# Performance work log

Hardware: AMD Instinct MI355X
Metric: run time of the kernel (lower is better)

Reference implementation:

```python
import jax, jax.numpy as jnp
import numpy as np

H = 1024
NS, NQ, S = 32, 64, 256
ADAPT_STEPS = 5


def _mlp_ln(x, W1, b1, W2, b2, g, be):
    # Linear -> ReLU -> Linear -> LayerNorm (dropout is identity in eval)
    h = jax.nn.relu(x @ W1 + b1) @ W2 + b2
    mu = h.mean(-1, keepdims=True)
    var = ((h - mu) ** 2).mean(-1, keepdims=True)
    return g * (h - mu) / jnp.sqrt(var + 1e-5) + be


def setup_inputs() -> dict:
    key = jax.random.key(0)
    ks = jax.random.split(key, 16)
    d = {}
    d['support_embeddings'] = jax.random.normal(ks[0], (NS, S, H), jnp.float32)
    d['query_embeddings'] = jax.random.normal(ks[1], (NQ, S, H), jnp.float32)
    d['support_labels'] = jax.random.randint(ks[2], (NS, S), 0, 3)
    w = lambda k, fi, fo: jax.random.normal(k, (fi, fo), jnp.float32) * (1.0 / np.sqrt(fi))
    # aspect_aware encoder
    d['aw_W1'] = w(ks[3], H, H); d['aw_b1'] = jnp.zeros((H,), jnp.float32)
    d['aw_W2'] = w(ks[4], H, H); d['aw_b2'] = jnp.zeros((H,), jnp.float32)
    d['aw_g'] = jnp.ones((H,), jnp.float32); d['aw_be'] = jnp.zeros((H,), jnp.float32)
    # aspect_contrastive encoder
    d['ct_W1'] = w(ks[5], H, H); d['ct_b1'] = jnp.zeros((H,), jnp.float32)
    d['ct_W2'] = w(ks[6], H, H); d['ct_b2'] = jnp.zeros((H,), jnp.float32)
    d['ct_g'] = jnp.ones((H,), jnp.float32); d['ct_be'] = jnp.zeros((H,), jnp.float32)
    # adaptation net (randomly-initialized 2-layer MLP in the torch code)
    d['ad_W1'] = w(ks[7], H, H); d['ad_b1'] = jnp.zeros((H,), jnp.float32)
    d['ad_W2'] = w(ks[8], H, H); d['ad_b2'] = jnp.zeros((H,), jnp.float32)
    # meta classifier
    d['cl_W1'] = w(ks[9], 2 * H, H); d['cl_b1'] = jnp.zeros((H,), jnp.float32)
    d['cl_W2'] = w(ks[10], H, 64); d['cl_b2'] = jnp.zeros((64,), jnp.float32)
    d['cl_W3'] = w(ks[11], 64, 3); d['cl_b3'] = jnp.zeros((3,), jnp.float32)
    return d


def reference(support_embeddings, query_embeddings, support_labels,
              aw_W1, aw_b1, aw_W2, aw_b2, aw_g, aw_be,
              ct_W1, ct_b1, ct_W2, ct_b2, ct_g, ct_be,
              ad_W1, ad_b1, ad_W2, ad_b2,
              cl_W1, cl_b1, cl_W2, cl_b2, cl_W3, cl_b3):
    # --- encode support set, build per-sentence aspect prototypes ---
    aw_s = _mlp_ln(support_embeddings, aw_W1, aw_b1, aw_W2, aw_b2, aw_g, aw_be)  # [NS,S,H]
    mask = (support_labels > 0).astype(aw_s.dtype)[..., None]                    # [NS,S,1]
    cnt = jnp.maximum(mask.sum(axis=1), 1.0)                                     # [NS,1]
    protos = (aw_s * mask).sum(axis=1) / cnt                                     # [NS,H] masked mean
    pn = protos / jnp.maximum(jnp.linalg.norm(protos, axis=-1, keepdims=True), 1e-8)

    # --- meta-adaptation: fused over all (query, token) pairs, 5 steps ---
    adapted = query_embeddings
    for _ in range(ADAPT_STEPS):
        qn = adapted / jnp.maximum(jnp.linalg.norm(adapted, axis=-1, keepdims=True), 1e-8)
        sims = jnp.einsum('qsh,ph->qsp', qn, pn)           # cosine similarities
        wts = jax.nn.softmax(sims, axis=-1)
        infl = jnp.einsum('qsp,ph->qsh', wts, protos)      # prototype influence
        adapted = jax.nn.relu((adapted + infl) @ ad_W1 + ad_b1) @ ad_W2 + ad_b2

    # --- classify adapted query tokens ---
    q_aw = _mlp_ln(adapted, aw_W1, aw_b1, aw_W2, aw_b2, aw_g, aw_be)
    q_ct = _mlp_ln(adapted, ct_W1, ct_b1, ct_W2, ct_b2, ct_g, ct_be)
    comb = jnp.concatenate([q_aw, q_ct], axis=-1)          # [NQ,S,2H]
    h = jax.nn.relu(comb @ cl_W1 + cl_b1)
    h = jax.nn.relu(h @ cl_W2 + cl_b2)
    preds = h @ cl_W3 + cl_b3                              # [NQ,S,3]
    return preds
```

## Files before the change

kernel.cpp:

```cpp
#include <hip/hip_runtime.h>
#include <hip/hip_bf16.h>

#define H 1024
#define NS 32
#define SS 256
#define T_Q 16384
#define M_S 8192

typedef __hip_bfloat16 bf16;
typedef short short8 __attribute__((ext_vector_type(8)));
typedef float floatx4 __attribute__((ext_vector_type(4)));

__device__ __forceinline__ float ldf(const bf16& v) { return __bfloat162float(v); }

__device__ __forceinline__ void split2(float v, bf16& h, bf16& l) {
  h = __float2bfloat16(v);
  l = __float2bfloat16(v - __bfloat162float(h));
}

__device__ __forceinline__ void gl2lds16(const void* g, void* l) {
  __builtin_amdgcn_global_load_lds(
      (const __attribute__((address_space(1))) unsigned int*)g,
      (__attribute__((address_space(3))) unsigned int*)l, 16, 0, 0);
}

__device__ __forceinline__ short8 ld8s(const bf16* p) { return *(const short8*)p; }

__global__ __launch_bounds__(256) void conv_split(const float* __restrict__ in,
                                                  bf16* __restrict__ oh,
                                                  bf16* __restrict__ ol, int n)
{
  int i = blockIdx.x * 256 + threadIdx.x;
  if (i < n) { bf16 h, l; split2(in[i], h, l); oh[i] = h; ol[i] = l; }
}

__global__ __launch_bounds__(256) void transpose_split(
    const float* __restrict__ W, bf16* __restrict__ Wh, bf16* __restrict__ Wl,
    int K, int N)
{
  __shared__ float t[32][33];
  int n0 = blockIdx.x * 32, k0 = blockIdx.y * 32;
  int tx = threadIdx.x & 31, ty = threadIdx.x >> 5;
#pragma unroll
  for (int i = 0; i < 32; i += 8)
    t[ty + i][tx] = W[(size_t)(k0 + ty + i) * N + (n0 + tx)];
  __syncthreads();
#pragma unroll
  for (int i = 0; i < 32; i += 8) {
    bf16 h, l; split2(t[tx][ty + i], h, l);
    size_t o = (size_t)(n0 + ty + i) * K + (k0 + tx);
    Wh[o] = h;
    if (Wl) Wl[o] = l;
  }
}

template<bool RELU, bool HASWL>
__global__ __launch_bounds__(512, 2) void gemm3p(
    const bf16* __restrict__ A0h, const bf16* __restrict__ A0l,
    const bf16* __restrict__ A1h, const bf16* __restrict__ A1l,
    const bf16* __restrict__ Wh,  const bf16* __restrict__ Wl,
    const float* __restrict__ bias,
    bf16* __restrict__ Ch, bf16* __restrict__ Cl,
    int M, int N, int K0, int Ktot)
{
  (void)M;
  __shared__ __align__(16) bf16 lds[2 * 32768];
  const int tid = threadIdx.x;
  const int w = tid >> 6, l = tid & 63;
  const int nbm = gridDim.x >> 2;
  const int lid = blockIdx.x;
  const int xcd = lid & 7, ib = lid >> 3;
  const int half = nbm >> 1;
  const int bn = xcd >> 1;
  const int bm = (xcd & 1) * half + ib;
  const int wr = w >> 2, wn = w & 3;
  const int m16 = l & 15, quad = l >> 4;
  const int srow = l & 15;
  const int scol = (l >> 4) * 8;
  const int la = l * 8;

  floatx4 acc[8][4];
#pragma unroll
  for (int i = 0; i < 8; i++)
#pragma unroll
    for (int j = 0; j < 4; j++) { acc[i][j][0]=0.f; acc[i][j][1]=0.f; acc[i][j][2]=0.f; acc[i][j][3]=0.f; }

  const size_t raB0 = (size_t)(bn * 256 + (2 * w)     * 16 + srow) * Ktot + scol;
  const size_t raB1 = (size_t)(bn * 256 + (2 * w + 1) * 16 + srow) * Ktot + scol;
  const int aT  = ((w >> 1) & 1) + ((w >> 1) >> 1) * 8;
  const int aLo = w & 1;
  const size_t raA = (size_t)(bm * 256 + aT * 16 + srow) * H + scol;
  const int aDst = (aLo ? 8192 : 0) + aT * 512;
  size_t raBt[3]; int bDst[3]; int bLo[3];
#pragma unroll
  for (int i = 0; i < 3; i++) {
    int j = w * 3 + i;
    int idx = j >> 1;
    int tb = (idx < 6) ? (idx + 2) : (idx + 4);
    bLo[i] = j & 1;
    raBt[i] = (size_t)(bm * 256 + tb * 16 + srow) * H + scol;
    bDst[i] = (bLo[i] ? 8192 : 0) + tb * 512;
  }

  auto stage_alpha = [&](int t) {
    const int k0 = t << 5;
    const bf16 *Ah_, *Al_; int ke;
    if (k0 < K0) { Ah_ = A0h; Al_ = A0l; ke = k0; }
    else         { Ah_ = A1h; Al_ = A1l; ke = k0 - K0; }
    bf16* buf = lds + (t & 1) * 32768;
    gl2lds16(Wh + raB0 + k0, buf + 16384 + (2 * w) * 512);
    gl2lds16(Wh + raB1 + k0, buf + 16384 + (2 * w + 1) * 512);
    if (HASWL) {
      gl2lds16(Wl + raB0 + k0, buf + 24576 + (2 * w) * 512);
      gl2lds16(Wl + raB1 + k0, buf + 24576 + (2 * w + 1) * 512);
    }
    gl2lds16((aLo ? Al_ : Ah_) + raA + ke, buf + aDst);
  };
  auto stage_beta = [&](int t) {
    const int k0 = t << 5;
    const bf16 *Ah_, *Al_; int ke;
    if (k0 < K0) { Ah_ = A0h; Al_ = A0l; ke = k0; }
    else         { Ah_ = A1h; Al_ = A1l; ke = k0 - K0; }
    bf16* buf = lds + (t & 1) * 32768;
#pragma unroll
    for (int i = 0; i < 3; i++)
      gl2lds16((bLo[i] ? Al_ : Ah_) + raBt[i] + ke, buf + bDst[i]);
  };

  stage_alpha(0);
  stage_beta(0);
  asm volatile("s_waitcnt vmcnt(0)" ::: "memory");
  __builtin_amdgcn_s_barrier();

  short8 bh[4], bl8[4];
  short8 s0h[2], s0l[2], s1h[2], s1l[2];
  {
    const bf16* bB = lds + 16384 + wn * 2048 + la;
#pragma unroll
    for (int nt = 0; nt < 4; nt++) bh[nt] = ld8s(bB + nt * 512);
    if (HASWL) {
#pragma unroll
      for (int nt = 0; nt < 4; nt++) bl8[nt] = ld8s(bB + 8192 + nt * 512);
    }
    const bf16* bA = lds + wr * 4096 + la;
    s0h[0] = ld8s(bA);        s0h[1] = ld8s(bA + 512);
    s0l[0] = ld8s(bA + 8192); s0l[1] = ld8s(bA + 8704);
  }

  const int nT = Ktot >> 5;

#define MM3(MI, AH, AL)                                                                            \
    _Pragma("unroll")                                                                              \
    for (int nt = 0; nt < 4; nt++) {                                                               \
      acc[MI][nt] = __builtin_amdgcn_mfma_f32_16x16x32_bf16(AH, bh[nt],  acc[MI][nt], 0, 0, 0);    \
      acc[MI][nt] = __builtin_amdgcn_mfma_f32_16x16x32_bf16(AL, bh[nt],  acc[MI][nt], 0, 0, 0);    \
      if (HASWL)                                                                                   \
        acc[MI][nt] = __builtin_amdgcn_mfma_f32_16x16x32_bf16(AH, bl8[nt], acc[MI][nt], 0, 0, 0);  \
    }

  for (int t = 0; t < nT; ++t) {
    const bf16* buf  = lds + (t & 1) * 32768;
    const bf16* nbuf = lds + ((t + 1) & 1) * 32768;
    const bf16* bA   = buf + wr * 4096 + la;
    const bf16* bAl  = bA + 8192;

    if (t + 1 < nT) stage_alpha(t + 1);
    s1h[0] = ld8s(bA + 1024);  s1h[1] = ld8s(bA + 1536);
    s1l[0] = ld8s(bAl + 1024); s1l[1] = ld8s(bAl + 1536);
    __builtin_amdgcn_s_setprio(1);
    MM3(0, s0h[0], s0l[0])
    MM3(1, s0h[1], s0l[1])
    __builtin_amdgcn_s_setprio(0);

    if (t + 1 < nT) stage_beta(t + 1);
    s0h[0] = ld8s(bA + 2048);  s0h[1] = ld8s(bA + 2560);
    s0l[0] = ld8s(bAl + 2048); s0l[1] = ld8s(bAl + 2560);
    __builtin_amdgcn_s_setprio(1);
    MM3(2, s1h[0], s1l[0])
    MM3(3, s1h[1], s1l[1])
    __builtin_amdgcn_s_setprio(0);

    s1h[0] = ld8s(bA + 3072);  s1h[1] = ld8s(bA + 3584);
    s1l[0] = ld8s(bAl + 3072); s1l[1] = ld8s(bAl + 3584);
    __builtin_amdgcn_s_setprio(1);
    MM3(4, s0h[0], s0l[0])
    MM3(5, s0h[1], s0l[1])
    __builtin_amdgcn_s_setprio(0);
    if (t + 1 < nT) asm volatile("s_waitcnt vmcnt(3)" ::: "memory");
    __builtin_amdgcn_s_barrier();

    __builtin_amdgcn_s_setprio(1);
    MM3(6, s1h[0], s1l[0])
    MM3(7, s1h[1], s1l[1])
    __builtin_amdgcn_s_setprio(0);
    if (t + 1 < nT) {
      const bf16* nbB = nbuf + 16384 + wn * 2048 + la;
      const bf16* nbA = nbuf + wr * 4096 + la;
#pragma unroll
      for (int nt = 0; nt < 4; nt++) bh[nt] = ld8s(nbB + nt * 512);
      if (HASWL) {
#pragma unroll
        for (int nt = 0; nt < 4; nt++) bl8[nt] = ld8s(nbB + 8192 + nt * 512);
      }
      s0h[0] = ld8s(nbA);        s0h[1] = ld8s(nbA + 512);
      s0l[0] = ld8s(nbA + 8192); s0l[1] = ld8s(nbA + 8704);
      asm volatile("s_waitcnt vmcnt(0)" ::: "memory");
    }
    __builtin_amdgcn_s_barrier();
  }
#undef MM3

#pragma unroll
  for (int mt = 0; mt < 8; mt++) {
#pragma unroll
    for (int nt = 0; nt < 4; nt++) {
      int row0 = bm * 256 + wr * 128 + mt * 16 + quad * 4;
      int col  = bn * 256 + wn * 64 + nt * 16 + m16;
      float bv = bias ? bias[col] : 0.f;
#pragma unroll
      for (int r = 0; r < 4; r++) {
        float v = acc[mt][nt][r] + bv;
        if (RELU) v = fmaxf(v, 0.f);
        bf16 h, lo; split2(v, h, lo);
        size_t o = (size_t)(row0 + r) * N + col;
        Ch[o] = h; Cl[o] = lo;
      }
    }
  }
}

__global__ __launch_bounds__(256) void ln_pair(
    bf16* __restrict__ hh, bf16* __restrict__ hl,
    const float* __restrict__ g, const float* __restrict__ be)
{
  int row = blockIdx.x;
  bf16* ph = hh + (size_t)row * H;
  bf16* pl = hl + (size_t)row * H;
  int tid = threadIdx.x;
  float v[4];
  float s = 0.f, sq = 0.f;
#pragma unroll
  for (int j = 0; j < 4; j++) {
    int hi = tid + 256 * j;
    v[j] = ldf(ph[hi]) + ldf(pl[hi]);
    s += v[j]; sq += v[j] * v[j];
  }
  __shared__ float rs[256], rq[256];
  rs[tid] = s; rq[tid] = sq; __syncthreads();
  for (int o = 128; o; o >>= 1) {
    if (tid < o) { rs[tid] += rs[tid + o]; rq[tid] += rq[tid + o]; }
    __syncthreads();
  }
  float mu   = rs[0] * (1.0f / H);
  float var  = rq[0] * (1.0f / H) - mu * mu;
  float rstd = rsqrtf(var + 1e-5f);
#pragma unroll
  for (int j = 0; j < 4; j++) {
    int hi = tid + 256 * j;
    bf16 h, l; split2(g[hi] * (v[j] - mu) * rstd + be[hi], h, l);
    ph[hi] = h; pl[hi] = l;
  }
}

__global__ __launch_bounds__(256) void proto_kernel(
    const bf16* __restrict__ eh, const bf16* __restrict__ el,
    const int* __restrict__ labels, float* __restrict__ protos_out)
{
  int p = blockIdx.x;
  int tid = threadIdx.x;
  __shared__ unsigned char lbl[SS];
  lbl[tid] = (labels[p * SS + tid] > 0) ? 1 : 0;
  __syncthreads();
  float acc[4] = {0.f, 0.f, 0.f, 0.f};
  int cnt = 0;
  const bf16* bh = eh + (size_t)p * SS * H;
  const bf16* bl = el + (size_t)p * SS * H;
  for (int s = 0; s < SS; s++) {
    if (lbl[s]) {
      cnt++;
      const bf16* rh = bh + (size_t)s * H;
      const bf16* rl = bl + (size_t)s * H;
#pragma unroll
      for (int j = 0; j < 4; j++)
        acc[j] += ldf(rh[tid + 256 * j]) + ldf(rl[tid + 256 * j]);
    }
  }
  float ic = 1.0f / fmaxf((float)cnt, 1.0f);
#pragma unroll
  for (int j = 0; j < 4; j++) protos_out[p * H + tid + 256 * j] = acc[j] * ic;
}

__global__ __launch_bounds__(256) void pn_kernel(
    const float* __restrict__ protos, bf16* __restrict__ pnh, bf16* __restrict__ pnl)
{
  int p = blockIdx.x;
  int tid = threadIdx.x;
  __shared__ float red[256];
  float v[4];
  float sq = 0.f;
#pragma unroll
  for (int j = 0; j < 4; j++) { v[j] = protos[p * H + tid + 256 * j]; sq += v[j] * v[j]; }
  red[tid] = sq; __syncthreads();
  for (int o = 128; o; o >>= 1) {
    if (tid < o) red[tid] += red[tid + o];
    __syncthreads();
  }
  float inv = 1.0f / fmaxf(sqrtf(red[0]), 1e-8f);
#pragma unroll
  for (int j = 0; j < 4; j++) {
    bf16 h, l; split2(v[j] * inv, h, l);
    pnh[p * H + tid + 256 * j] = h;
    pnl[p * H + tid + 256 * j] = l;
  }
}

__global__ __launch_bounds__(256) void rownorm_pair(
    const bf16* __restrict__ hh, const bf16* __restrict__ hl, float* __restrict__ rn)
{
  int row = blockIdx.x;
  int tid = threadIdx.x;
  const bf16* ph = hh + (size_t)row * H;
  const bf16* pl = hl + (size_t)row * H;
  float s = 0.f;
#pragma unroll
  for (int j = 0; j < 4; j++) {
    float v = ldf(ph[tid + 256 * j]) + ldf(pl[tid + 256 * j]);
    s += v * v;
  }
  __shared__ float rs[256];
  rs[tid] = s; __syncthreads();
  for (int o = 128; o; o >>= 1) {
    if (tid < o) rs[tid] += rs[tid + o];
    __syncthreads();
  }
  if (tid == 0) rn[row] = 1.0f / fmaxf(sqrtf(rs[0]), 1e-8f);
}

__global__ __launch_bounds__(256) void sims_mfma(
    const bf16* __restrict__ Ah, const bf16* __restrict__ Al,
    const bf16* __restrict__ Bh, const bf16* __restrict__ Bl,
    float* __restrict__ sims)
{
  __shared__ bf16 AsH[64 * 32];
  __shared__ bf16 AsL[64 * 32];
  __shared__ bf16 BsH[32 * 32];
  __shared__ bf16 BsL[32 * 32];
  const int tid = threadIdx.x;
  const int w = tid >> 6, l = tid & 63;
  const int bm0 = blockIdx.x * 64;
  const int m16 = l & 15, quad = l >> 4;
  const int sr = l >> 2;
  const int sc = (l & 3) * 8;

  floatx4 acc[2];
#pragma unroll
  for (int nt = 0; nt < 2; nt++) { acc[nt][0]=0.f; acc[nt][1]=0.f; acc[nt][2]=0.f; acc[nt][3]=0.f; }

  for (int k0 = 0; k0 < H; k0 += 32) {
    gl2lds16(Ah + (size_t)(bm0 + w * 16 + sr) * H + k0 + sc, &AsH[w * 512]);
    gl2lds16(Al + (size_t)(bm0 + w * 16 + sr) * H + k0 + sc, &AsL[w * 512]);
    if (w < 2) gl2lds16(Bh + (size_t)(w * 16 + sr) * H + k0 + sc, &BsH[w * 512]);
    else       gl2lds16(Bl + (size_t)((w - 2) * 16 + sr) * H + k0 + sc, &BsL[(w - 2) * 512]);
    __syncthreads();

    short8 ah  = *(const short8*)&AsH[(w * 16 + m16) * 32 + quad * 8];
    short8 al8 = *(const short8*)&AsL[(w * 16 + m16) * 32 + quad * 8];
#pragma unroll
    for (int nt = 0; nt < 2; nt++) {
      short8 bh  = *(const short8*)&BsH[(nt * 16 + m16) * 32 + quad * 8];
      short8 bl8 = *(const short8*)&BsL[(nt * 16 + m16) * 32 + quad * 8];
      acc[nt] = __builtin_amdgcn_mfma_f32_16x16x32_bf16(ah,  bh,  acc[nt], 0, 0, 0);
      acc[nt] = __builtin_amdgcn_mfma_f32_16x16x32_bf16(al8, bh,  acc[nt], 0, 0, 0);
      acc[nt] = __builtin_amdgcn_mfma_f32_16x16x32_bf16(ah,  bl8, acc[nt], 0, 0, 0);
    }
    __syncthreads();
  }

#pragma unroll
  for (int nt = 0; nt < 2; nt++) {
    int col  = nt * 16 + m16;
    int row0 = bm0 + w * 16 + quad * 4;
#pragma unroll
    for (int r = 0; r < 4; r++)
      sims[(size_t)(row0 + r) * 32 + col] = acc[nt][r];
  }
}

__global__ __launch_bounds__(256) void softmax32(
    const float* __restrict__ sims, const float* __restrict__ rn,
    float* __restrict__ wts)
{
  int t = blockIdx.x * 8 + (threadIdx.x >> 5);
  int p = threadIdx.x & 31;
  float s = sims[(size_t)t * 32 + p] * rn[t];
  float m = s;
#pragma unroll
  for (int o = 16; o; o >>= 1) m = fmaxf(m, __shfl_xor(m, o, 64));
  float e = __expf(s - m);
  float sum = e;
#pragma unroll
  for (int o = 16; o; o >>= 1) sum += __shfl_xor(sum, o, 64);
  wts[(size_t)t * 32 + p] = e / sum;
}

__global__ __launch_bounds__(256) void infl16(
    const bf16* __restrict__ ah, const bf16* __restrict__ al,
    const float* __restrict__ wts, const float* __restrict__ protos,
    bf16* __restrict__ oh, bf16* __restrict__ ol)
{
  int t0 = blockIdx.x * 16;
  int tid = threadIdx.x;
  __shared__ float wl[16][32];
  for (int i = tid; i < 512; i += 256)
    wl[i >> 5][i & 31] = wts[(size_t)(t0 + (i >> 5)) * 32 + (i & 31)];
  __syncthreads();
  int c0 = tid * 4;
  float acc[16][4];
#pragma unroll
  for (int tk = 0; tk < 16; tk++) {
    const bf16* rh = ah + (size_t)(t0 + tk) * H + c0;
    const bf16* rl = al + (size_t)(t0 + tk) * H + c0;
#pragma unroll
    for (int j = 0; j < 4; j++) acc[tk][j] = ldf(rh[j]) + ldf(rl[j]);
  }
  for (int p = 0; p < 32; p++) {
    float4 pv = *(const float4*)&protos[p * H + c0];
#pragma unroll
    for (int tk = 0; tk < 16; tk++) {
      float w = wl[tk][p];
      acc[tk][0] += w * pv.x; acc[tk][1] += w * pv.y;
      acc[tk][2] += w * pv.z; acc[tk][3] += w * pv.w;
    }
  }
#pragma unroll
  for (int tk = 0; tk < 16; tk++) {
    bf16* wh = oh + (size_t)(t0 + tk) * H + c0;
    bf16* wo = ol + (size_t)(t0 + tk) * H + c0;
#pragma unroll
    for (int j = 0; j < 4; j++) { bf16 h, lo; split2(acc[tk][j], h, lo); wh[j] = h; wo[j] = lo; }
  }
}

__global__ __launch_bounds__(256) void gemm_small(
    const bf16* __restrict__ Ah, const bf16* __restrict__ Al,
    const float* __restrict__ W, const float* __restrict__ bias,
    float* __restrict__ C, int M, int N, int K)
{
  const int BK = 16;
  __shared__ float As[BK][64];
  __shared__ float Bs[BK][64];
  int tid = threadIdx.x;
  int tx = tid & 15, ty = tid >> 4;
  int bn0 = blockIdx.x * 64;
  int bm0 = blockIdx.y * 64;
  float acc[4][4] = {};
  int am = tid >> 2, ak = (tid & 3) * 4;
  int bk = tid >> 4, bn = (tid & 15) * 4;
  const bf16* Aph = Ah + (size_t)(bm0 + am) * K + ak;
  const bf16* Apl = Al + (size_t)(bm0 + am) * K + ak;
  const float* Wptr = W + (size_t)bk * N + bn0 + bn;
  for (int k0 = 0; k0 < K; k0 += BK) {
#pragma unroll
    for (int c = 0; c < 4; c++) As[ak + c][am] = ldf(Aph[c]) + ldf(Apl[c]);
#pragma unroll
    for (int c = 0; c < 4; c++) Bs[bk][bn + c] = Wptr[c];
    __syncthreads();
#pragma unroll
    for (int k = 0; k < BK; k++) {
      float a[4], b[4];
#pragma unroll
      for (int i = 0; i < 4; i++) a[i] = As[k][ty * 4 + i];
#pragma unroll
      for (int j = 0; j < 4; j++) b[j] = Bs[k][tx * 4 + j];
#pragma unroll
      for (int i = 0; i < 4; i++)
#pragma unroll
        for (int j = 0; j < 4; j++)
          acc[i][j] += a[i] * b[j];
    }
    __syncthreads();
    Aph += BK; Apl += BK;
    Wptr += (size_t)BK * N;
  }
#pragma unroll
  for (int i = 0; i < 4; i++) {
    float* Crow = C + (size_t)(bm0 + ty * 4 + i) * N + bn0;
#pragma unroll
    for (int j = 0; j < 4; j++) {
      int n = tx * 4 + j;
      Crow[n] = fmaxf(acc[i][j] + bias[bn0 + n], 0.f);
    }
  }
}

__global__ __launch_bounds__(256) void FewShotABSALearner_46935402610855_kernel(
    const float* __restrict__ h2, const float* __restrict__ W3,
    const float* __restrict__ b3, float* __restrict__ out,
    int t0, int nElem, int out_size)
{
  int idx = blockIdx.x * 256 + threadIdx.x;
  if (idx >= nElem) return;
  int t = idx / 3, c = idx - t * 3;
  float acc = b3[c];
  const float* hr = h2 + (size_t)t * 64;
#pragma unroll
  for (int k = 0; k < 64; k++) acc += hr[k] * W3[k * 3 + c];
  int oi = t0 * 3 + idx;
  if (oi < out_size) out[oi] = acc;
}

extern "C" void kernel_launch(void* const* d_in, const int* in_sizes, int n_in,
                              void* d_out, int out_size, void* d_ws, size_t ws_size,
                              hipStream_t stream)
{
  (void)in_sizes; (void)n_in;
  const float* sup   = (const float*)d_in[0];
  const float* qry   = (const float*)d_in[1];
  const int*   lab   = (const int*)d_in[2];
  const float *aw_W1 = (const float*)d_in[3],  *aw_b1 = (const float*)d_in[4];
  const float *aw_W2 = (const float*)d_in[5],  *aw_b2 = (const float*)d_in[6];
  const float *aw_g  = (const float*)d_in[7],  *aw_be = (const float*)d_in[8];
  const float *ct_W1 = (const float*)d_in[9],  *ct_b1 = (const float*)d_in[10];
  const float *ct_W2 = (const float*)d_in[11], *ct_b2 = (const float*)d_in[12];
  const float *ct_g  = (const float*)d_in[13], *ct_be = (const float*)d_in[14];
  const float *ad_W1 = (const float*)d_in[15], *ad_b1 = (const float*)d_in[16];
  const float *ad_W2 = (const float*)d_in[17], *ad_b2 = (const float*)d_in[18];
  const float *cl_W1 = (const float*)d_in[19], *cl_b1 = (const float*)d_in[20];
  const float *cl_W2 = (const float*)d_in[21], *cl_b2 = (const float*)d_in[22];
  const float *cl_W3 = (const float*)d_in[23], *cl_b3 = (const float*)d_in[24];
  float* out = (float*)d_out;

  const size_t MB = 1 << 20;
  int C; bool clLo = true;
  if      (ws_size >= (size_t)239403008) C = 16384;
  else if (ws_size >= (size_t)136609792) C = 8192;
  else if (ws_size >= (size_t)85213184)  C = 4096;
  else if (ws_size >= (size_t)59514880)  C = 2048;
  else if (ws_size >= (size_t)46665728)  C = 1024;
  else { C = 1024; clLo = false; }
  const int Cs = (C < M_S) ? C : M_S;
  const size_t actB = (size_t)C * H * sizeof(bf16);

  char* ws = (char*)d_ws;
  size_t off = 0;
  auto nxt = [&](size_t b) { char* p = ws + off; off += b; return p; };
  bf16* sqw[12];
  for (int i = 0; i < 12; i++) sqw[i] = (bf16*)nxt(2 * MB);
  bf16 *aw1h = sqw[0], *aw1l = sqw[1], *aw2h = sqw[2],  *aw2l = sqw[3];
  bf16 *ct1h = sqw[4], *ct1l = sqw[5], *ct2h = sqw[6],  *ct2l = sqw[7];
  bf16 *ad1h = sqw[8], *ad1l = sqw[9], *ad2h = sqw[10], *ad2l = sqw[11];
  bf16* clW1h = (bf16*)nxt(4 * MB);
  bf16* clW1l = clLo ? (bf16*)nxt(4 * MB) : nullptr;
  float* protos = (float*)nxt(NS * H * 4);
  bf16*  pnh    = (bf16*)nxt(NS * H * 2);
  bf16*  pnl    = (bf16*)nxt(NS * H * 2);
  char*  ub     = nxt((size_t)C * 256);
  float* h2c   = (float*)ub;
  float* simsb = (float*)ub;
  float* wtsb  = (float*)(ub + (size_t)C * 128);
  float* rn    = (float*)nxt((size_t)C * 4);
  bf16 *R0h = (bf16*)nxt(actB), *R0l = (bf16*)nxt(actB);
  bf16 *R1h = (bf16*)nxt(actB), *R1l = (bf16*)nxt(actB);
  bf16 *R2h = (bf16*)nxt(actB), *R2l = (bf16*)nxt(actB);

  dim3 blk(256);
  dim3 blk2(512);
  dim3 tg(32, 32);
  dim3 ggq((C / 256) * 4);
  dim3 ggs((Cs / 256) * 4);

  transpose_split<<<tg, blk, 0, stream>>>(aw_W1, aw1h, aw1l, H, H);
  transpose_split<<<tg, blk, 0, stream>>>(aw_W2, aw2h, aw2l, H, H);
  transpose_split<<<tg, blk, 0, stream>>>(ct_W1, ct1h, ct1l, H, H);
  transpose_split<<<tg, blk, 0, stream>>>(ct_W2, ct2h, ct2l, H, H);
  transpose_split<<<tg, blk, 0, stream>>>(ad_W1, ad1h, ad1l, H, H);
  transpose_split<<<tg, blk, 0, stream>>>(ad_W2, ad2h, ad2l, H, H);
  transpose_split<<<dim3(32, 64), blk, 0, stream>>>(cl_W1, clW1h, clW1l, 2 * H, H);

  for (int sc = 0; sc < M_S / Cs; sc++) {
    conv_split<<<(Cs * H) / 256, blk, 0, stream>>>(sup + (size_t)sc * Cs * H, R0h, R0l, Cs * H);
    gemm3p<true , true><<<ggs, blk2, 0, stream>>>(R0h, R0l, R0h, R0l, aw1h, aw1l, aw_b1, R1h, R1l, Cs, H, H, H);
    gemm3p<false, true><<<ggs, blk2, 0, stream>>>(R1h, R1l, R1h, R1l, aw2h, aw2l, aw_b2, R2h, R2l, Cs, H, H, H);
    ln_pair<<<Cs, blk, 0, stream>>>(R2h, R2l, aw_g, aw_be);
    proto_kernel<<<Cs / SS, blk, 0, stream>>>(R2h, R2l, lab + sc * Cs,
                                              protos + (size_t)sc * (Cs / SS) * H);
  }
  pn_kernel<<<NS, blk, 0, stream>>>(protos, pnh, pnl);

  for (int qc = 0; qc < T_Q / C; qc++) {
    const float* q0 = qry + (size_t)qc * C * H;
    conv_split<<<(C * H) / 256, blk, 0, stream>>>(q0, R2h, R2l, C * H);
    for (int it = 0; it < 5; it++) {
      rownorm_pair<<<C, blk, 0, stream>>>(R2h, R2l, rn);
      sims_mfma<<<C / 64, blk, 0, stream>>>(R2h, R2l, pnh, pnl, simsb);
      softmax32<<<C / 8, blk, 0, stream>>>(simsb, rn, wtsb);
      infl16<<<C / 16, blk, 0, stream>>>(R2h, R2l, wtsb, protos, R0h, R0l);
      gemm3p<true , true><<<ggq, blk2, 0, stream>>>(R0h, R0l, R0h, R0l, ad1h, ad1l, ad_b1, R1h, R1l, C, H, H, H);
      gemm3p<false, true><<<ggq, blk2, 0, stream>>>(R1h, R1l, R1h, R1l, ad2h, ad2l, ad_b2, R2h, R2l, C, H, H, H);
    }
    gemm3p<true , true><<<ggq, blk2, 0, stream>>>(R2h, R2l, R2h, R2l, aw1h, aw1l, aw_b1, R0h, R0l, C, H, H, H);
    gemm3p<false, true><<<ggq, blk2, 0, stream>>>(R0h, R0l, R0h, R0l, aw2h, aw2l, aw_b2, R1h, R1l, C, H, H, H);
    ln_pair<<<C, blk, 0, stream>>>(R1h, R1l, aw_g, aw_be);
    gemm3p<true , true><<<ggq, blk2, 0, stream>>>(R2h, R2l, R2h, R2l, ct1h, ct1l, ct_b1, R0h, R0l, C, H, H, H);
    gemm3p<false, true><<<ggq, blk2, 0, stream>>>(R0h, R0l, R0h, R0l, ct2h, ct2l, ct_b2, R2h, R2l, C, H, H, H);
    ln_pair<<<C, blk, 0, stream>>>(R2h, R2l, ct_g, ct_be);
    if (clLo)
      gemm3p<true, true ><<<ggq, blk2, 0, stream>>>(R1h, R1l, R2h, R2l, clW1h, clW1l, cl_b1, R0h, R0l, C, H, H, 2 * H);
    else
      gemm3p<true, false><<<ggq, blk2, 0, stream>>>(R1h, R1l, R2h, R2l, clW1h, nullptr, cl_b1, R0h, R0l, C, H, H, 2 * H);
    gemm_small<<<dim3(1, C / 64), blk, 0, stream>>>(R0h, R0l, cl_W2, cl_b2, h2c, C, 64, H);
    FewShotABSALearner_46935402610855_kernel<<<(C * 3 + 255) / 256, blk, 0, stream>>>(
        h2c, cl_W3, cl_b3, out, qc * C, C * 3, out_size);
  }
}
```

Before: 2.422 ms.

## Switch GEMM inner loop from 16x16x32 to 32x32x16 bf16 MFMA tiles

Replaces the 16x16x32 MFMA tiling with 32x32x16 MFMA instructions. The LDS fragment addressing, register fragments, accumulator layout (4x2 floatx16) and epilogue row/column mapping are all reworked to match. Larger MFMA tiles cut the number of LDS fragment reads per FLOP and the instruction-issue overhead. The cost is a different LDS access pattern that may bank-conflict, and a more scattered store pattern in the epilogue.

After: 2.486 ms. 1.03x slower.

```diff
diff --git a/kernel.cpp b/kernel.cpp
--- a/kernel.cpp
+++ b/kernel.cpp
@@ -10,6 +10,7 @@
 typedef __hip_bfloat16 bf16;
 typedef short short8 __attribute__((ext_vector_type(8)));
 typedef float floatx4 __attribute__((ext_vector_type(4)));
+typedef float floatx16 __attribute__((ext_vector_type(16)));
 
 __device__ __forceinline__ float ldf(const bf16& v) { return __bfloat162float(v); }
 
@@ -74,16 +75,17 @@
   const int bn = xcd >> 1;
   const int bm = (xcd & 1) * half + ib;
   const int wr = w >> 2, wn = w & 3;
-  const int m16 = l & 15, quad = l >> 4;
   const int srow = l & 15;
   const int scol = (l >> 4) * 8;
-  const int la = l * 8;
-
-  floatx4 acc[8][4];
-#pragma unroll
-  for (int i = 0; i < 8; i++)
-#pragma unroll
-    for (int j = 0; j < 4; j++) { acc[i][j][0]=0.f; acc[i][j][1]=0.f; acc[i][j][2]=0.f; acc[i][j][3]=0.f; }
+  const int fb = (((l & 31) >> 4) << 9) + ((l >> 5) << 7) + ((l & 15) << 3);
+
+  floatx16 acc[4][2];
+#pragma unroll
+  for (int i = 0; i < 4; i++)
+#pragma unroll
+    for (int j = 0; j < 2; j++)
+#pragma unroll
+      for (int r = 0; r < 16; r++) acc[i][j][r] = 0.f;
 
   const size_t raB0 = (size_t)(bn * 256 + (2 * w)     * 16 + srow) * Ktot + scol;
   const size_t raB1 = (size_t)(bn * 256 + (2 * w + 1) * 16 + srow) * Ktot + scol;
@@ -132,97 +134,102 @@
   asm volatile("s_waitcnt vmcnt(0)" ::: "memory");
   __builtin_amdgcn_s_barrier();
 
-  short8 bh[4], bl8[4];
+  short8 Bh0[2], Bh1[2], Bl0[2], Bl1[2];
   short8 s0h[2], s0l[2], s1h[2], s1l[2];
   {
-    const bf16* bB = lds + 16384 + wn * 2048 + la;
-#pragma unroll
-    for (int nt = 0; nt < 4; nt++) bh[nt] = ld8s(bB + nt * 512);
+    const bf16* pB = lds + 16384 + wn * 2048 + fb;
+    Bh0[0] = ld8s(pB);         Bh0[1] = ld8s(pB + 1024);
+    Bh1[0] = ld8s(pB + 256);   Bh1[1] = ld8s(pB + 1024 + 256);
     if (HASWL) {
-#pragma unroll
-      for (int nt = 0; nt < 4; nt++) bl8[nt] = ld8s(bB + 8192 + nt * 512);
-    }
-    const bf16* bA = lds + wr * 4096 + la;
-    s0h[0] = ld8s(bA);        s0h[1] = ld8s(bA + 512);
-    s0l[0] = ld8s(bA + 8192); s0l[1] = ld8s(bA + 8704);
+      Bl0[0] = ld8s(pB + 8192);        Bl0[1] = ld8s(pB + 8192 + 1024);
+      Bl1[0] = ld8s(pB + 8192 + 256);  Bl1[1] = ld8s(pB + 8192 + 1024 + 256);
+    }
+    const bf16* pA = lds + wr * 4096 + fb;
+    s0h[0] = ld8s(pA);         s0l[0] = ld8s(pA + 8192);
   }
 
   const int nT = Ktot >> 5;
 
-#define MM3(MI, AH, AL)                                                                            \
-    _Pragma("unroll")                                                                              \
-    for (int nt = 0; nt < 4; nt++) {                                                               \
-      acc[MI][nt] = __builtin_amdgcn_mfma_f32_16x16x32_bf16(AH, bh[nt],  acc[MI][nt], 0, 0, 0);    \
-      acc[MI][nt] = __builtin_amdgcn_mfma_f32_16x16x32_bf16(AL, bh[nt],  acc[MI][nt], 0, 0, 0);    \
-      if (HASWL)                                                                                   \
-        acc[MI][nt] = __builtin_amdgcn_mfma_f32_16x16x32_bf16(AH, bl8[nt], acc[MI][nt], 0, 0, 0);  \
-    }
+#define MM32(AT, BT, BH, BL, AH, AL)                                                               \
+    acc[AT][BT] = __builtin_amdgcn_mfma_f32_32x32x16_bf16(AH, BH, acc[AT][BT], 0, 0, 0);           \
+    acc[AT][BT] = __builtin_amdgcn_mfma_f32_32x32x16_bf16(AL, BH, acc[AT][BT], 0, 0, 0);           \
+    if (HASWL)                                                                                     \
+      acc[AT][BT] = __builtin_amdgcn_mfma_f32_32x32x16_bf16(AH, BL, acc[AT][BT], 0, 0, 0);
 
   for (int t = 0; t < nT; ++t) {
     const bf16* buf  = lds + (t & 1) * 32768;
     const bf16* nbuf = lds + ((t + 1) & 1) * 32768;
-    const bf16* bA   = buf + wr * 4096 + la;
-    const bf16* bAl  = bA + 8192;
-
+    const bf16* pA   = buf + wr * 4096 + fb;
+    const bf16* pAl  = pA + 8192;
+
+    s0h[1] = ld8s(pA + 1024);   s0l[1] = ld8s(pAl + 1024);
     if (t + 1 < nT) stage_alpha(t + 1);
-    s1h[0] = ld8s(bA + 1024);  s1h[1] = ld8s(bA + 1536);
-    s1l[0] = ld8s(bAl + 1024); s1l[1] = ld8s(bAl + 1536);
+    s1h[0] = ld8s(pA + 2048);   s1h[1] = ld8s(pA + 3072);
+    s1l[0] = ld8s(pAl + 2048);  s1l[1] = ld8s(pAl + 3072);
     __builtin_amdgcn_s_setprio(1);
-    MM3(0, s0h[0], s0l[0])
-    MM3(1, s0h[1], s0l[1])
+    MM32(0, 0, Bh0[0], Bl0[0], s0h[0], s0l[0])
+    MM32(0, 1, Bh0[1], Bl0[1], s0h[0], s0l[0])
+    MM32(1, 0, Bh0[0], Bl0[0], s0h[1], s0l[1])
+    MM32(1, 1, Bh0[1], Bl0[1], s0h[1], s0l[1])
     __builtin_amdgcn_s_setprio(0);
 
     if (t + 1 < nT) stage_beta(t + 1);
-    s0h[0] = ld8s(bA + 2048);  s0h[1] = ld8s(bA + 2560);
-    s0l[0] = ld8s(bAl + 2048); s0l[1] = ld8s(bAl + 2560);
+    s0h[0] = ld8s(pA + 256);          s0h[1] = ld8s(pA + 1024 + 256);
+    s0l[0] = ld8s(pAl + 256);         s0l[1] = ld8s(pAl + 1024 + 256);
     __builtin_amdgcn_s_setprio(1);
-    MM3(2, s1h[0], s1l[0])
-    MM3(3, s1h[1], s1l[1])
+    MM32(2, 0, Bh0[0], Bl0[0], s1h[0], s1l[0])
+    MM32(2, 1, Bh0[1], Bl0[1], s1h[0], s1l[0])
+    MM32(3, 0, Bh0[0], Bl0[0], s1h[1], s1l[1])
+    MM32(3, 1, Bh0[1], Bl0[1], s1h[1], s1l[1])
     __builtin_amdgcn_s_setprio(0);
 
-    s1h[0] = ld8s(bA + 3072);  s1h[1] = ld8s(bA + 3584);
-    s1l[0] = ld8s(bAl + 3072); s1l[1] = ld8s(bAl + 3584);
+    s1h[0] = ld8s(pA + 2048 + 256);   s1h[1] = ld8s(pA + 3072 + 256);
+    s1l[0] = ld8s(pAl + 2048 + 256);  s1l[1] = ld8s(pAl + 3072 + 256);
     __builtin_amdgcn_s_setprio(1);
-    MM3(4, s0h[0], s0l[0])
-    MM3(5, s0h[1], s0l[1])
+    MM32(0, 0, Bh1[0], Bl1[0], s0h[0], s0l[0])
+    MM32(0, 1, Bh1[1], Bl1[1], s0h[0], s0l[0])
+    MM32(1, 0, Bh1[0], Bl1[0], s0h[1], s0l[1])
+    MM32(1, 1, Bh1[1], Bl1[1], s0h[1], s0l[1])
     __builtin_amdgcn_s_setprio(0);
     if (t + 1 < nT) asm volatile("s_waitcnt vmcnt(3)" ::: "memory");
     __builtin_amdgcn_s_barrier();
 
     __builtin_amdgcn_s_setprio(1);
-    MM3(6, s1h[0], s1l[0])
-    MM3(7, s1h[1], s1l[1])
+    MM32(2, 0, Bh1[0], Bl1[0], s1h[0], s1l[0])
+    MM32(2, 1, Bh1[1], Bl1[1], s1h[0], s1l[0])
+    MM32(3, 0, Bh1[0], Bl1[0], s1h[1], s1l[1])
+    MM32(3, 1, Bh1[1], Bl1[1], s1h[1], s1l[1])
     __builtin_amdgcn_s_setprio(0);
     if (t + 1 < nT) {
-      const bf16* nbB = nbuf + 16384 + wn * 2048 + la;
-      const bf16* nbA = nbuf + wr * 4096 + la;
-#pragma unroll
-      for (int nt = 0; nt < 4; nt++) bh[nt] = ld8s(nbB + nt * 512);
+      const bf16* nB = nbuf + 16384 + wn * 2048 + fb;
+      const bf16* nA = nbuf + wr * 4096 + fb;
+      Bh0[0] = ld8s(nB);         Bh0[1] = ld8s(nB + 1024);
+      Bh1[0] = ld8s(nB + 256);   Bh1[1] = ld8s(nB + 1024 + 256);
       if (HASWL) {
-#pragma unroll
-        for (int nt = 0; nt < 4; nt++) bl8[nt] = ld8s(nbB + 8192 + nt * 512);
+        Bl0[0] = ld8s(nB + 8192);        Bl0[1] = ld8s(nB + 8192 + 1024);
+        Bl1[0] = ld8s(nB + 8192 + 256);  Bl1[1] = ld8s(nB + 8192 + 1024 + 256);
       }
-      s0h[0] = ld8s(nbA);        s0h[1] = ld8s(nbA + 512);
-      s0l[0] = ld8s(nbA + 8192); s0l[1] = ld8s(nbA + 8704);
+      s0h[0] = ld8s(nA);         s0l[0] = ld8s(nA + 8192);
       asm volatile("s_waitcnt vmcnt(0)" ::: "memory");
     }
     __builtin_amdgcn_s_barrier();
   }
-#undef MM3
-
-#pragma unroll
-  for (int mt = 0; mt < 8; mt++) {
-#pragma unroll
-    for (int nt = 0; nt < 4; nt++) {
-      int row0 = bm * 256 + wr * 128 + mt * 16 + quad * 4;
-      int col  = bn * 256 + wn * 64 + nt * 16 + m16;
+#undef MM32
+
+#pragma unroll
+  for (int at = 0; at < 4; at++) {
+#pragma unroll
+    for (int bt = 0; bt < 2; bt++) {
+      int col  = bn * 256 + wn * 64 + bt * 32 + (l & 31);
+      int row0 = bm * 256 + wr * 128 + at * 32 + 4 * (l >> 5);
       float bv = bias ? bias[col] : 0.f;
 #pragma unroll
-      for (int r = 0; r < 4; r++) {
-        float v = acc[mt][nt][r] + bv;
+      for (int r = 0; r < 16; r++) {
+        int row = row0 + (r & 3) + 8 * (r >> 2);
+        float v = acc[at][bt][r] + bv;
         if (RELU) v = fmaxf(v, 0.f);
         bf16 h, lo; split2(v, h, lo);
-        size_t o = (size_t)(row0 + r) * N + col;
+        size_t o = (size_t)row * N + col;
         Ch[o] = h; Cl[o] = lo;
       }
     }
```
